# Kernel tuning notes

Measured on AMD Instinct MI355X. Metric: run time of the kernel, lower is better.

Reference implementation:

```python
import jax, jax.numpy as jnp
import numpy as np

S, B, E, H = 2048, 4, 1024, 16
D = E // H


def setup_inputs() -> dict:
    key = jax.random.key(0)
    ks = jax.random.split(key, 12)
    scale = 1.0 / np.sqrt(E)
    inp = {
        "query": jax.random.normal(ks[0], (S, B, E), jnp.float32),
        "key": jax.random.normal(ks[1], (S, B, E), jnp.float32),
        "value": jax.random.normal(ks[2], (S, B, E), jnp.float32),
        # causal mask: True = masked out (matches masked_fill semantics)
        "attn_mask": jnp.triu(jnp.ones((S, S), jnp.bool_), k=1),
        "Wq": jax.random.normal(ks[3], (E, E), jnp.float32) * scale,
        "bq": jax.random.normal(ks[4], (E,), jnp.float32) * scale,
        "Wk": jax.random.normal(ks[5], (E, E), jnp.float32) * scale,
        "bk": jax.random.normal(ks[6], (E,), jnp.float32) * scale,
        "Wv": jax.random.normal(ks[7], (E, E), jnp.float32) * scale,
        "bv": jax.random.normal(ks[8], (E,), jnp.float32) * scale,
        "Wo": jax.random.normal(ks[9], (E, E), jnp.float32) * scale,
        "bo": jax.random.normal(ks[10], (E,), jnp.float32) * scale,
    }
    return inp


def reference(query, key, value, attn_mask, Wq, bq, Wk, bk, Wv, bv, Wo, bo):
    # inputs are [S, B, E]; torch Linear: y = x @ W.T + b
    def proj_heads(x, W, b):
        y = jnp.einsum("sbe,fe->sbf", x, W) + b          # [S,B,E]
        return y.transpose(1, 0, 2).reshape(B, S, H, D).transpose(0, 2, 1, 3)  # [B,H,S,D]

    Q = proj_heads(query, Wq, bq)
    K = proj_heads(key, Wk, bk)
    V = proj_heads(value, Wv, bv)

    scores = jnp.einsum("bhsd,bhtd->bhst", Q, K) / jnp.sqrt(jnp.float32(D))
    scores = jnp.where(attn_mask[None, None, :, :], -jnp.inf, scores)
    probs = jax.nn.softmax(scores, axis=-1)              # dropout p=0 -> identity

    ctx = jnp.einsum("bhst,bhtd->bhsd", probs, V)        # [B,H,S,D]
    ctx = ctx.transpose(0, 2, 1, 3).reshape(B, S, E).transpose(1, 0, 2)  # [S,B,E]

    out = jnp.einsum("sbe,fe->sbf", ctx, Wo) + bo        # [S,B,E]
    attn_map = probs.mean(axis=1)                        # [B,S,S]
    return out, attn_map
```

## Files before the change

kernel.cpp:

```cpp
#include <hip/hip_runtime.h>
#include <stdint.h>

#define S_LEN 2048
#define B_SZ  4
#define E_SZ  1024
#define H_CNT 16
#define D_HD  64

typedef __attribute__((ext_vector_type(4))) float          f32x4;
typedef __attribute__((ext_vector_type(2))) float          f32x2;
typedef __attribute__((ext_vector_type(8))) __bf16         bf16x8;
typedef __attribute__((ext_vector_type(4))) unsigned short u16x4;
typedef __attribute__((ext_vector_type(4))) int            i32x4;
typedef __attribute__((ext_vector_type(2))) int            i32x2;
typedef unsigned short us;

#define QSCALE 0.1803368801111204f

__device__ __forceinline__ us bfu(float f) {
    __bf16 h = (__bf16)f;
    return __builtin_bit_cast(us, h);
}
__device__ __forceinline__ unsigned pk2(float a, float b) {
    return (unsigned)bfu(a) | ((unsigned)bfu(b) << 16);
}
#define EXP2(x) __builtin_amdgcn_exp2f(x)
#define MFMA(a, b, c) __builtin_amdgcn_mfma_f32_16x16x32_bf16((a), (b), (c), 0, 0, 0)

__device__ __forceinline__ void gll16(const void* g, void* l) {
    __builtin_amdgcn_global_load_lds(
        (const __attribute__((address_space(1))) void*)g,
        (__attribute__((address_space(3))) void*)l, 16, 0, 0);
}

__global__ __launch_bounds__(256)
void convert_many(const float* __restrict__ s0, const float* __restrict__ s1,
                  const float* __restrict__ s2, const float* __restrict__ s3,
                  us* __restrict__ d0, us* __restrict__ d1,
                  us* __restrict__ d2, us* __restrict__ d3,
                  float sc0)
{
    const int which = blockIdx.y;
    const float* s = which == 0 ? s0 : which == 1 ? s1 : which == 2 ? s2 : s3;
    us* d = which == 0 ? d0 : which == 1 ? d1 : which == 2 ? d2 : d3;
    const float sc = which == 0 ? sc0 : 1.0f;
    const int i = blockIdx.x * 256 + threadIdx.x;
    f32x4 v = ((const f32x4*)s)[i];
    u16x4 o;
    o.x = bfu(v.x * sc); o.y = bfu(v.y * sc);
    o.z = bfu(v.z * sc); o.w = bfu(v.w * sc);
    ((u16x4*)d)[i] = o;
}

template<bool AF32, bool OUT_QKV>
__global__ __launch_bounds__(256)
void gemm_bt(const void* __restrict__ Ap,
             const us* __restrict__ Bw,
             const float* __restrict__ bias, float bscale,
             void* __restrict__ Outp)
{
    __shared__ us Al[2][128 * 64];
    __shared__ us Bl[2][128 * 64];

    const int t     = threadIdx.x;
    const int lane  = t & 63;
    const int wave  = t >> 6;
    const int lrow  = lane & 15;
    const int lk    = lane >> 4;
    const int xq    = blockIdx.x & 7;
    const int kq    = blockIdx.x >> 3;
    const int bm    = ((kq & 56) | xq) << 7;
    const int bn    = (kq & 7) << 7;
    const int wr    = (wave >> 1) << 6;
    const int wc    = (wave & 1) << 6;
    const int srow8 = lane >> 3;
    const int scol  = (lane & 7) << 3;

    f32x4 acc[4][4];
    #pragma unroll
    for (int i = 0; i < 4; ++i)
        #pragma unroll
        for (int j = 0; j < 4; ++j) acc[i][j] = (f32x4)0.0f;

    #define GSTAGE(k0_, dst_)                                                        \
        _Pragma("unroll")                                                            \
        for (int j_ = 0; j_ < 4; ++j_) {                                             \
            const int chunk_ = wave * 4 + j_;                                        \
            const int r_ = chunk_ * 8 + srow8;                                       \
            gll16((const us*)Ap + (size_t)(bm + r_) * E_SZ + (k0_) + scol,           \
                  &Al[dst_][chunk_ * 512]);                                          \
            gll16(Bw + (size_t)(bn + r_) * E_SZ + (k0_) + scol,                      \
                  &Bl[dst_][chunk_ * 512]);                                          \
        }

    #define GCOMP(src_)                                                              \
        _Pragma("unroll")                                                            \
        for (int kk = 0; kk < 2; ++kk) {                                             \
            bf16x8 af[4], bfr[4];                                                    \
            _Pragma("unroll")                                                        \
            for (int i = 0; i < 4; ++i)                                              \
                af[i] = *(const bf16x8*)(&Al[src_][(wr + i*16 + lrow) * 64 + kk*32 + lk*8]); \
            _Pragma("unroll")                                                        \
            for (int j = 0; j < 4; ++j)                                              \
                bfr[j] = *(const bf16x8*)(&Bl[src_][(wc + j*16 + lrow) * 64 + kk*32 + lk*8]); \
            _Pragma("unroll")                                                        \
            for (int i = 0; i < 4; ++i)                                              \
                _Pragma("unroll")                                                    \
                for (int j = 0; j < 4; ++j)                                          \
                    acc[i][j] = MFMA(af[i], bfr[j], acc[i][j]);                      \
        }

    if (AF32) {
        for (int k0 = 0; k0 < E_SZ; k0 += 64) {
            __syncthreads();
            #pragma unroll
            for (int j = 0; j < 4; ++j) {
                const int chunk = wave * 4 + j;
                const int r = chunk * 8 + srow8;
                const float* ga = (const float*)Ap + (size_t)(bm + r) * E_SZ + k0 + scol;
                f32x4 u0 = *(const f32x4*)ga;
                f32x4 u1 = *(const f32x4*)(ga + 4);
                i32x4 wv;
                wv.x = (int)pk2(u0.x, u0.y); wv.y = (int)pk2(u0.z, u0.w);
                wv.z = (int)pk2(u1.x, u1.y); wv.w = (int)pk2(u1.z, u1.w);
                *(i32x4*)(&Al[0][chunk * 512 + lane * 8]) = wv;
                gll16(Bw + (size_t)(bn + r) * E_SZ + k0 + scol, &Bl[0][chunk * 512]);
            }
            __syncthreads();
            GCOMP(0);
        }
    } else {
        GSTAGE(0, 0);
        __syncthreads();
        int buf = 0;
        #pragma unroll 2
        for (int kt = 0; kt < 15; ++kt) {
            GSTAGE((kt + 1) * 64, buf ^ 1);
            GCOMP(buf);
            __syncthreads();
            buf ^= 1;
        }
        GCOMP(buf);
    }
    #undef GSTAGE
    #undef GCOMP

    const int crow = lk << 2;
    #pragma unroll
    for (int i = 0; i < 4; ++i) {
        #pragma unroll
        for (int j = 0; j < 4; ++j) {
            const int n = bn + wc + j*16 + lrow;
            const float bv = bias[n] * bscale;
            #pragma unroll
            for (int r = 0; r < 4; ++r) {
                const int m = bm + wr + i*16 + crow + r;
                const float val = acc[i][j][r] + bv;
                if (OUT_QKV) {
                    const int s = m >> 2, b = m & 3;
                    const int h = n >> 6, d = n & 63;
                    ((us*)Outp)[((size_t)(b*H_CNT + h)*S_LEN + s)*D_HD + d] = bfu(val);
                } else {
                    ((float*)Outp)[(size_t)m * E_SZ + n] = val;
                }
            }
        }
    }
}

__global__ __launch_bounds__(512, 6)
void flash_fwd(const us* __restrict__ Qb,
               const us* __restrict__ Kb,
               const us* __restrict__ Vb,
               us* __restrict__ ctx,
               float* __restrict__ mout,
               float* __restrict__ lout)
{
    __shared__ us Kl[2][64 * 64];
    __shared__ us Vt[2][64 * 72];
    __shared__ us Pl[8][16 * 72];

    const int t    = threadIdx.x;
    const int lane = t & 63, wave = t >> 6;
    const int lrow = lane & 15, lk = lane >> 4;
    const int bh   = blockIdx.x & 63;
    const int qt   = 15 - (blockIdx.x >> 6);
    const int b    = bh >> 4, h = bh & 15;

    const size_t base = (size_t)bh * S_LEN * D_HD;
    const us* Q = Qb + base;
    const us* K = Kb + base;
    const us* V = Vb + base;

    const int qbase = qt * 128 + wave * 16;
    const int myq   = qbase + lrow;
    us* pl = &Pl[wave][0];

    bf16x8 qf[2];
    #pragma unroll
    for (int ks = 0; ks < 2; ++ks)
        qf[ks] = *(const bf16x8*)(Q + (size_t)myq * D_HD + ks*32 + lk*8);

    f32x4 ctxa[4];
    #pragma unroll
    for (int nf = 0; nf < 4; ++nf) ctxa[nf] = (f32x4)0.0f;
    float mst = -__builtin_inff(), lst = 0.0f;

    const int tU  = t & 255;
    const int vp2 = (tU & 31) << 1;
    const int vd8 = (tU >> 5) << 3;

    i32x4 v0, v1;

    #define STAGE_K(kv_, kl_)                                                        \
        if (t < 256) {                                                               \
            _Pragma("unroll")                                                        \
            for (int i_ = 0; i_ < 2; ++i_) {                                         \
                const int row_  = i_*32 + (t >> 3);                                  \
                const int slot_ = (t & 7) ^ (row_ & 7);                              \
                gll16(K + (size_t)((kv_) + row_)*D_HD + slot_*8,                     \
                      (kl_) + i_*2048 + ((t >> 6) << 9));                            \
            }                                                                        \
        }
    #define LOAD_V(kv_)                                                             \
        if (t >= 256) {                                                              \
            const us* vp_ = V + (size_t)((kv_) + vp2)*D_HD + vd8;                    \
            v0 = *(const i32x4*)vp_;                                                 \
            v1 = *(const i32x4*)(vp_ + D_HD);                                        \
        }
    #define WRITE_V(vt_)                                                             \
        if (t >= 256) {                                                              \
            union { i32x4 v; us s[8]; } ua_, ub_; ua_.v = v0; ub_.v = v1;            \
            _Pragma("unroll")                                                        \
            for (int j_ = 0; j_ < 8; ++j_) {                                         \
                unsigned w_ = (unsigned)ua_.s[j_] | ((unsigned)ub_.s[j_] << 16);     \
                *(unsigned*)((vt_) + (vd8 + j_)*72 + vp2) = w_;                      \
            }                                                                        \
        }

    STAGE_K(0, Kl[0]);
    LOAD_V(0);
    WRITE_V(Vt[0]);
    __syncthreads();

    const int kvend = qt*128 + 128;
    int cur = 0;
    for (int kv = 0; kv < kvend; kv += 64) {
        const bool more = (kv + 64) < kvend;
        if (more) {
            STAGE_K(kv + 64, Kl[cur ^ 1]);
            LOAD_V(kv + 64);
        }

        if (kv <= qbase) {
            const us* kl = Kl[cur];
            const us* vt = Vt[cur];
            f32x4 sa[4];
            #pragma unroll
            for (int nf = 0; nf < 4; ++nf) sa[nf] = (f32x4)0.0f;
            #pragma unroll
            for (int ks = 0; ks < 2; ++ks)
                #pragma unroll
                for (int nf = 0; nf < 4; ++nf) {
                    const int key = nf*16 + lrow;
                    bf16x8 kf = *(const bf16x8*)((const char*)kl + (key << 7) +
                                    (((((ks << 2) | lk)) ^ (lrow & 7)) << 4));
                    sa[nf] = MFMA(kf, qf[ks], sa[nf]);
                }
            if (kv + 63 > qbase) {
                #pragma unroll
                for (int nf = 0; nf < 4; ++nf)
                    #pragma unroll
                    for (int r = 0; r < 4; ++r)
                        if (kv + nf*16 + (lk << 2) + r > myq) sa[nf][r] = -__builtin_inff();
            }
            float pmax = sa[0][0];
            #pragma unroll
            for (int nf = 0; nf < 4; ++nf)
                #pragma unroll
                for (int r = 0; r < 4; ++r) pmax = fmaxf(pmax, sa[nf][r]);
            pmax = fmaxf(pmax, __shfl_xor(pmax, 16));
            pmax = fmaxf(pmax, __shfl_xor(pmax, 32));
            const bool skip = __all(pmax <= mst + 8.0f);
            if (!skip) {
                const float mnew  = fmaxf(mst, pmax);
                const float alpha = EXP2(mst - mnew);
                mst = mnew;
                lst *= alpha;
                float ar[4];
                #pragma unroll
                for (int r = 0; r < 4; ++r) ar[r] = __shfl(alpha, (lk << 2) + r);
                #pragma unroll
                for (int nf = 0; nf < 4; ++nf)
                    #pragma unroll
                    for (int r = 0; r < 4; ++r) ctxa[nf][r] *= ar[r];
            }
            float sum = 0.0f;
            #pragma unroll
            for (int nf = 0; nf < 4; ++nf)
                #pragma unroll
                for (int r = 0; r < 4; ++r) {
                    const float p = EXP2(sa[nf][r] - mst);
                    sa[nf][r] = p;
                    sum += p;
                }
            sum += __shfl_xor(sum, 16);
            sum += __shfl_xor(sum, 32);
            lst += sum;
            #pragma unroll
            for (int nf = 0; nf < 4; ++nf) {
                i32x2 dw;
                dw.x = (int)pk2(sa[nf][0], sa[nf][1]);
                dw.y = (int)pk2(sa[nf][2], sa[nf][3]);
                *(i32x2*)(pl + lrow*72 + nf*16 + (lk << 2)) = dw;
            }
            #pragma unroll
            for (int ks = 0; ks < 2; ++ks) {
                bf16x8 pa = *(const bf16x8*)(pl + lrow*72 + ks*32 + lk*8);
                #pragma unroll
                for (int nf = 0; nf < 4; ++nf) {
                    bf16x8 vf = *(const bf16x8*)(vt + (nf*16 + lrow)*72 + ks*32 + lk*8);
                    ctxa[nf] = MFMA(pa, vf, ctxa[nf]);
                }
            }
        }

        if (more) { WRITE_V(Vt[cur ^ 1]); }
        __syncthreads();
        cur ^= 1;
    }

    const float inv = 1.0f / lst;
    float invr[4];
    #pragma unroll
    for (int r = 0; r < 4; ++r) invr[r] = __shfl(inv, (lk << 2) + r);
    #pragma unroll
    for (int nf = 0; nf < 4; ++nf)
        #pragma unroll
        for (int r = 0; r < 4; ++r) {
            const int srow = qbase + (lk << 2) + r;
            const int d    = nf*16 + lrow;
            ctx[((size_t)srow * B_SZ + b) * E_SZ + h*D_HD + d] = bfu(ctxa[nf][r] * invr[r]);
        }
    if (lane < 16) {
        mout[(size_t)bh * S_LEN + myq] = mst;
        lout[(size_t)bh * S_LEN + myq] = inv * 0.0625f;
    }
    #undef STAGE_K
    #undef LOAD_V
    #undef WRITE_V
}

__global__ __launch_bounds__(512, 4)
void attn_map_k(const us* __restrict__ Qb,
                const us* __restrict__ Kb,
                const float* __restrict__ mrows,
                const float* __restrict__ lrows,
                float* __restrict__ map)
{
    const int t  = threadIdx.x;
    const int xq = blockIdx.x & 7;
    const int rq = blockIdx.x >> 3;
    const int p  = ((rq >> 4) << 3) | xq;
    const int jt = rq & 15;
    const int it = p & 15;
    const int b  = p >> 4;
    float* mt = map + ((size_t)b * S_LEN + it*128) * S_LEN + jt*128;

    if (jt > it) {
        f32x4 z = (f32x4)0.0f;
        #pragma unroll
        for (int i = 0; i < 8; ++i) {
            const int c = i*512 + t;
            *(f32x4*)(mt + (size_t)(c >> 5) * S_LEN + (c & 31) * 4) = z;
        }
        return;
    }

    __shared__ us Ql[128 * 64];
    __shared__ us Kl[128 * 64];
    __shared__ f32x2 Mll[16 * 128];

    const int lane = t & 63, wave = t >> 6;
    const int lrow = lane & 15, lk = lane >> 4;
    const int wr = (wave >> 1) << 5;
    const int wc = (wave & 1) << 6;

    #pragma unroll
    for (int i = 0; i < 4; ++i) {
        const int idx = i*512 + t;
        const int h = idx >> 7, row = idx & 127;
        f32x2 v;
        v.x = mrows[(size_t)(b*H_CNT + h)*S_LEN + it*128 + row];
        v.y = lrows[(size_t)(b*H_CNT + h)*S_LEN + it*128 + row];
        Mll[idx] = v;
    }

    f32x4 pacc[2][4];
    #pragma unroll
    for (int i = 0; i < 2; ++i)
        #pragma unroll
        for (int j = 0; j < 4; ++j) pacc[i][j] = (f32x4)0.0f;

    const int qrow  = it*128;
    const int krow  = jt*128;
    const int srow  = t >> 3;
    const int sslot = t & 7;

    for (int h = 0; h < H_CNT; ++h) {
        const size_t base = (size_t)(b*H_CNT + h) * S_LEN * D_HD;
        const us* Qh = Qb + base + (size_t)qrow * D_HD;
        const us* Kh = Kb + base + (size_t)krow * D_HD;
        __syncthreads();
        #pragma unroll
        for (int i = 0; i < 2; ++i) {
            const int row  = i*64 + srow;
            const int slot = sslot ^ (row & 7);
            gll16(Qh + (size_t)row * D_HD + slot*8, &Ql[i*4096 + ((t >> 6) << 9)]);
            gll16(Kh + (size_t)row * D_HD + slot*8, &Kl[i*4096 + ((t >> 6) << 9)]);
        }
        __syncthreads();

        bf16x8 kf[4][2];
        #pragma unroll
        for (int nf = 0; nf < 4; ++nf)
            #pragma unroll
            for (int ks = 0; ks < 2; ++ks) {
                const int row = wc + nf*16 + lrow;
                kf[nf][ks] = *(const bf16x8*)(&Kl[row*64 + (((ks<<2)|lk) ^ (row&7))*8]);
            }

        #pragma unroll
        for (int mf = 0; mf < 2; ++mf) {
            const int arow = wr + mf*16 + lrow;
            bf16x8 af0 = *(const bf16x8*)(&Ql[arow*64 + ((lk)     ^ (arow&7))*8]);
            bf16x8 af1 = *(const bf16x8*)(&Ql[arow*64 + ((4 | lk) ^ (arow&7))*8]);
            f32x2 ml[4];
            #pragma unroll
            for (int r = 0; r < 4; ++r)
                ml[r] = Mll[h*128 + wr + mf*16 + (lk << 2) + r];
            #pragma unroll
            for (int nf = 0; nf < 4; ++nf) {
                f32x4 sa = (f32x4)0.0f;
                sa = MFMA(af0, kf[nf][0], sa);
                sa = MFMA(af1, kf[nf][1], sa);
                #pragma unroll
                for (int r = 0; r < 4; ++r)
                    pacc[mf][nf][r] += EXP2(sa[r] - ml[r].x) * ml[r].y;
            }
        }
    }

    #pragma unroll
    for (int mf = 0; mf < 2; ++mf)
        #pragma unroll
        for (int nf = 0; nf < 4; ++nf)
            #pragma unroll
            for (int r = 0; r < 4; ++r) {
                const int row = wr + mf*16 + (lk << 2) + r;
                const int col = wc + nf*16 + lrow;
                float v = pacc[mf][nf][r];
                if (it == jt && col > row) v = 0.0f;
                mt[(size_t)row * S_LEN + col] = v;
            }
}

extern "C" void kernel_launch(void* const* d_in, const int* in_sizes, int n_in,
                              void* d_out, int out_size, void* d_ws, size_t ws_size,
                              hipStream_t stream)
{
    const float* q_in = (const float*)d_in[0];
    const float* k_in = (const float*)d_in[1];
    const float* v_in = (const float*)d_in[2];
    const float* Wq = (const float*)d_in[4];
    const float* bq = (const float*)d_in[5];
    const float* Wk = (const float*)d_in[6];
    const float* bk = (const float*)d_in[7];
    const float* Wv = (const float*)d_in[8];
    const float* bv = (const float*)d_in[9];
    const float* Wo = (const float*)d_in[10];
    const float* bo = (const float*)d_in[11];

    const size_t EE   = (size_t)E_SZ * E_SZ;
    const size_t BHSD = (size_t)B_SZ * H_CNT * S_LEN * D_HD;
    const size_t SBE  = (size_t)S_LEN * B_SZ * E_SZ;

    us* Wqb = (us*)d_ws;
    us* Wkb = Wqb + EE;
    us* Wvb = Wkb + EE;
    us* Wob = Wvb + EE;
    us* base = Wob + EE;

    const size_t need_big = (4*EE + 6*BHSD) * sizeof(us);
    const bool big = ws_size >= need_big;

    us *Aq, *Ak, *Av, *Qb, *Kb, *Vb, *ctx;
    float* ml;
    if (big) {
        Aq = base;       Ak = Aq + BHSD;  Av = Ak + BHSD;
        Qb = Av + BHSD;  Kb = Qb + BHSD;  Vb = Kb + BHSD;
        ctx = Aq;
        ml  = (float*)Ak;
    } else {
        Aq = Ak = Av = nullptr;
        Qb = base;       Kb = Qb + BHSD;  Vb = Kb + BHSD;
        ctx = Vb + BHSD;
        ml  = (float*)(ctx + SBE);
    }
    float* mrows = ml;
    float* lrows = ml + (size_t)B_SZ * H_CNT * S_LEN;

    float* out = (float*)d_out;
    float* map = out + SBE;

    convert_many<<<dim3(1024, 4), 256, 0, stream>>>(Wq, Wk, Wv, Wo, Wqb, Wkb, Wvb, Wob, QSCALE);

    if (big) {
        convert_many<<<dim3(8192, 3), 256, 0, stream>>>(q_in, k_in, v_in, nullptr,
                                                        Aq, Ak, Av, nullptr, 1.0f);
        gemm_bt<false, true><<<512, 256, 0, stream>>>(Aq, Wqb, bq, QSCALE, Qb);
        gemm_bt<false, true><<<512, 256, 0, stream>>>(Ak, Wkb, bk, 1.0f,   Kb);
        gemm_bt<false, true><<<512, 256, 0, stream>>>(Av, Wvb, bv, 1.0f,   Vb);
    } else {
        gemm_bt<true, true><<<512, 256, 0, stream>>>(q_in, Wqb, bq, QSCALE, Qb);
        gemm_bt<true, true><<<512, 256, 0, stream>>>(k_in, Wkb, bk, 1.0f,   Kb);
        gemm_bt<true, true><<<512, 256, 0, stream>>>(v_in, Wvb, bv, 1.0f,   Vb);
    }

    flash_fwd<<<1024, 512, 0, stream>>>(Qb, Kb, Vb, ctx, mrows, lrows);

    gemm_bt<false, false><<<512, 256, 0, stream>>>(ctx, Wob, bo, 1.0f, d_out);

    attn_map_k<<<B_SZ*16*16, 512, 0, stream>>>(Qb, Kb, mrows, lrows, map);
}
```

Baseline: 255.4 us.

## Double-buffer fp32-input GEMM and attention-map head loop, drop separate input convert

The fp32-A GEMM path now prefetches the next K-tile into registers and a second LDS buffer while computing the current one, replacing the previous single-buffered load/sync/compute loop. The attention-map kernel double-buffers its per-head Q/K tiles, so loading the next head overlaps with the MFMA and exp work on the current head. The launcher always uses the fused fp32->bf16 conversion inside the projection GEMMs and drops the separate input-convert pass, which saves a full read/write of the inputs but makes GEMM A loads fp32 and register-staged. The extra LDS and registers may lower occupancy.

```diff
diff --git a/kernel.cpp b/kernel.cpp
--- a/kernel.cpp
+++ b/kernel.cpp
@@ -82,15 +82,42 @@
         #pragma unroll
         for (int j = 0; j < 4; ++j) acc[i][j] = (f32x4)0.0f;
 
-    #define GSTAGE(k0_, dst_)                                                        \
+    #define BSTAGE(k0_, dst_)                                                        \
+        _Pragma("unroll")                                                            \
+        for (int j_ = 0; j_ < 4; ++j_) {                                             \
+            const int chunk_ = wave * 4 + j_;                                        \
+            const int r_ = chunk_ * 8 + srow8;                                       \
+            gll16(Bw + (size_t)(bn + r_) * E_SZ + (k0_) + scol,                      \
+                  &Bl[dst_][chunk_ * 512]);                                          \
+        }
+
+    #define ASTAGE_G(k0_, dst_)                                                      \
         _Pragma("unroll")                                                            \
         for (int j_ = 0; j_ < 4; ++j_) {                                             \
             const int chunk_ = wave * 4 + j_;                                        \
             const int r_ = chunk_ * 8 + srow8;                                       \
             gll16((const us*)Ap + (size_t)(bm + r_) * E_SZ + (k0_) + scol,           \
                   &Al[dst_][chunk_ * 512]);                                          \
-            gll16(Bw + (size_t)(bn + r_) * E_SZ + (k0_) + scol,                      \
-                  &Bl[dst_][chunk_ * 512]);                                          \
+        }
+
+    #define ALOAD(k0_)                                                               \
+        _Pragma("unroll")                                                            \
+        for (int j_ = 0; j_ < 4; ++j_) {                                             \
+            const float* ga_ = (const float*)Ap +                                    \
+                (size_t)(bm + (wave*4 + j_)*8 + srow8) * E_SZ + (k0_) + scol;        \
+            au0[j_] = *(const f32x4*)ga_;                                            \
+            au1[j_] = *(const f32x4*)(ga_ + 4);                                      \
+        }
+
+    #define AWRITE(dst_)                                                             \
+        _Pragma("unroll")                                                            \
+        for (int j_ = 0; j_ < 4; ++j_) {                                             \
+            i32x4 wv_;                                                               \
+            wv_.x = (int)pk2(au0[j_].x, au0[j_].y);                                  \
+            wv_.y = (int)pk2(au0[j_].z, au0[j_].w);                                  \
+            wv_.z = (int)pk2(au1[j_].x, au1[j_].y);                                  \
+            wv_.w = (int)pk2(au1[j_].z, au1[j_].w);                                  \
+            *(i32x4*)(&Al[dst_][(wave*4 + j_) * 512 + lane * 8]) = wv_;              \
         }
 
     #define GCOMP(src_)                                                              \
@@ -111,38 +138,37 @@
         }
 
     if (AF32) {
-        for (int k0 = 0; k0 < E_SZ; k0 += 64) {
+        f32x4 au0[4], au1[4];
+        ALOAD(0); BSTAGE(0, 0); AWRITE(0);
+        __syncthreads();
+        int buf = 0;
+        for (int kt = 0; kt < 15; ++kt) {
+            ALOAD((kt + 1) * 64);
+            BSTAGE((kt + 1) * 64, buf ^ 1);
+            GCOMP(buf);
+            AWRITE(buf ^ 1);
             __syncthreads();
-            #pragma unroll
-            for (int j = 0; j < 4; ++j) {
-                const int chunk = wave * 4 + j;
-                const int r = chunk * 8 + srow8;
-                const float* ga = (const float*)Ap + (size_t)(bm + r) * E_SZ + k0 + scol;
-                f32x4 u0 = *(const f32x4*)ga;
-                f32x4 u1 = *(const f32x4*)(ga + 4);
-                i32x4 wv;
-                wv.x = (int)pk2(u0.x, u0.y); wv.y = (int)pk2(u0.z, u0.w);
-                wv.z = (int)pk2(u1.x, u1.y); wv.w = (int)pk2(u1.z, u1.w);
-                *(i32x4*)(&Al[0][chunk * 512 + lane * 8]) = wv;
-                gll16(Bw + (size_t)(bn + r) * E_SZ + k0 + scol, &Bl[0][chunk * 512]);
-            }
-            __syncthreads();
-            GCOMP(0);
-        }
+            buf ^= 1;
+        }
+        GCOMP(buf);
     } else {
-        GSTAGE(0, 0);
+        ASTAGE_G(0, 0); BSTAGE(0, 0);
         __syncthreads();
         int buf = 0;
         #pragma unroll 2
         for (int kt = 0; kt < 15; ++kt) {
-            GSTAGE((kt + 1) * 64, buf ^ 1);
+            ASTAGE_G((kt + 1) * 64, buf ^ 1);
+            BSTAGE((kt + 1) * 64, buf ^ 1);
             GCOMP(buf);
             __syncthreads();
             buf ^= 1;
         }
         GCOMP(buf);
     }
-    #undef GSTAGE
+    #undef BSTAGE
+    #undef ASTAGE_G
+    #undef ALOAD
+    #undef AWRITE
     #undef GCOMP
 
     const int crow = lk << 2;
@@ -377,8 +403,8 @@
         return;
     }
 
-    __shared__ us Ql[128 * 64];
-    __shared__ us Kl[128 * 64];
+    __shared__ us Ql[2][128 * 64];
+    __shared__ us Kl[2][128 * 64];
     __shared__ f32x2 Mll[16 * 128];
 
     const int lane = t & 63, wave = t >> 6;
@@ -407,34 +433,44 @@
     const int srow  = t >> 3;
     const int sslot = t & 7;
 
+    #define MSTAGE(h_, dst_)                                                         \
+        {                                                                            \
+            const size_t base_ = (size_t)(b*H_CNT + (h_)) * S_LEN * D_HD;            \
+            const us* Qh_ = Qb + base_ + (size_t)qrow * D_HD;                        \
+            const us* Kh_ = Kb + base_ + (size_t)krow * D_HD;                        \
+            _Pragma("unroll")                                                        \
+            for (int i_ = 0; i_ < 2; ++i_) {                                         \
+                const int row_  = i_*64 + srow;                                      \
+                const int slot_ = sslot ^ (row_ & 7);                                \
+                gll16(Qh_ + (size_t)row_ * D_HD + slot_*8,                           \
+                      &Ql[dst_][i_*4096 + ((t >> 6) << 9)]);                         \
+                gll16(Kh_ + (size_t)row_ * D_HD + slot_*8,                           \
+                      &Kl[dst_][i_*4096 + ((t >> 6) << 9)]);                         \
+            }                                                                        \
+        }
+
+    MSTAGE(0, 0);
+    __syncthreads();
+    int buf = 0;
     for (int h = 0; h < H_CNT; ++h) {
-        const size_t base = (size_t)(b*H_CNT + h) * S_LEN * D_HD;
-        const us* Qh = Qb + base + (size_t)qrow * D_HD;
-        const us* Kh = Kb + base + (size_t)krow * D_HD;
-        __syncthreads();
-        #pragma unroll
-        for (int i = 0; i < 2; ++i) {
-            const int row  = i*64 + srow;
-            const int slot = sslot ^ (row & 7);
-            gll16(Qh + (size_t)row * D_HD + slot*8, &Ql[i*4096 + ((t >> 6) << 9)]);
-            gll16(Kh + (size_t)row * D_HD + slot*8, &Kl[i*4096 + ((t >> 6) << 9)]);
-        }
-        __syncthreads();
-
+        if (h < H_CNT - 1) MSTAGE(h + 1, buf ^ 1);
+
+        const us* ql = Ql[buf];
+        const us* klp = Kl[buf];
         bf16x8 kf[4][2];
         #pragma unroll
         for (int nf = 0; nf < 4; ++nf)
             #pragma unroll
             for (int ks = 0; ks < 2; ++ks) {
                 const int row = wc + nf*16 + lrow;
-                kf[nf][ks] = *(const bf16x8*)(&Kl[row*64 + (((ks<<2)|lk) ^ (row&7))*8]);
+                kf[nf][ks] = *(const bf16x8*)(&klp[row*64 + (((ks<<2)|lk) ^ (row&7))*8]);
             }
 
         #pragma unroll
         for (int mf = 0; mf < 2; ++mf) {
             const int arow = wr + mf*16 + lrow;
-            bf16x8 af0 = *(const bf16x8*)(&Ql[arow*64 + ((lk)     ^ (arow&7))*8]);
-            bf16x8 af1 = *(const bf16x8*)(&Ql[arow*64 + ((4 | lk) ^ (arow&7))*8]);
+            bf16x8 af0 = *(const bf16x8*)(&ql[arow*64 + ((lk)     ^ (arow&7))*8]);
+            bf16x8 af1 = *(const bf16x8*)(&ql[arow*64 + ((4 | lk) ^ (arow&7))*8]);
             f32x2 ml[4];
             #pragma unroll
             for (int r = 0; r < 4; ++r)
@@ -449,7 +485,10 @@
                     pacc[mf][nf][r] += EXP2(sa[r] - ml[r].x) * ml[r].y;
             }
         }
-    }
+        __syncthreads();
+        buf ^= 1;
+    }
+    #undef MSTAGE
 
     #pragma unroll
     for (int mf = 0; mf < 2; ++mf)
@@ -489,43 +528,21 @@
     us* Wkb = Wqb + EE;
     us* Wvb = Wkb + EE;
     us* Wob = Wvb + EE;
-    us* base = Wob + EE;
-
-    const size_t need_big = (4*EE + 6*BHSD) * sizeof(us);
-    const bool big = ws_size >= need_big;
-
-    us *Aq, *Ak, *Av, *Qb, *Kb, *Vb, *ctx;
-    float* ml;
-    if (big) {
-        Aq = base;       Ak = Aq + BHSD;  Av = Ak + BHSD;
-        Qb = Av + BHSD;  Kb = Qb + BHSD;  Vb = Kb + BHSD;
-        ctx = Aq;
-        ml  = (float*)Ak;
-    } else {
-        Aq = Ak = Av = nullptr;
-        Qb = base;       Kb = Qb + BHSD;  Vb = Kb + BHSD;
-        ctx = Vb + BHSD;
-        ml  = (float*)(ctx + SBE);
-    }
-    float* mrows = ml;
-    float* lrows = ml + (size_t)B_SZ * H_CNT * S_LEN;
+    us* Qb  = Wob + EE;
+    us* Kb  = Qb + BHSD;
+    us* Vb  = Kb + BHSD;
+    us* ctx = Vb + BHSD;
+    float* mrows = (float*)(ctx + SBE);
+    float* lrows = mrows + (size_t)B_SZ * H_CNT * S_LEN;
 
     float* out = (float*)d_out;
     float* map = out + SBE;
 
     convert_many<<<dim3(1024, 4), 256, 0, stream>>>(Wq, Wk, Wv, Wo, Wqb, Wkb, Wvb, Wob, QSCALE);
 
-    if (big) {
-        convert_many<<<dim3(8192, 3), 256, 0, stream>>>(q_in, k_in, v_in, nullptr,
-                                                        Aq, Ak, Av, nullptr, 1.0f);
-        gemm_bt<false, true><<<512, 256, 0, stream>>>(Aq, Wqb, bq, QSCALE, Qb);
-        gemm_bt<false, true><<<512, 256, 0, stream>>>(Ak, Wkb, bk, 1.0f,   Kb);
-        gemm_bt<false, true><<<512, 256, 0, stream>>>(Av, Wvb, bv, 1.0f,   Vb);
-    } else {
-        gemm_bt<true, true><<<512, 256, 0, stream>>>(q_in, Wqb, bq, QSCALE, Qb);
-        gemm_bt<true, true><<<512, 256, 0, stream>>>(k_in, Wkb, bk, 1.0f,   Kb);
-        gemm_bt<true, true><<<512, 256, 0, stream>>>(v_in, Wvb, bv, 1.0f,   Vb);
-    }
+    gemm_bt<true, true><<<512, 256, 0, stream>>>(q_in, Wqb, bq, QSCALE, Qb);
+    gemm_bt<true, true><<<512, 256, 0, stream>>>(k_in, Wkb, bk, 1.0f,   Kb);
+    gemm_bt<true, true><<<512, 256, 0, stream>>>(v_in, Wvb, bv, 1.0f,   Vb);
 
     flash_fwd<<<1024, 512, 0, stream>>>(Qb, Kb, Vb, ctx, mrows, lrows);
 
```

New measurement: 285.5 us. 11.8% more time.
